# Performance work log

Measured on AMD Instinct MI355X. Metric: run time of the kernel, lower is better.

Reference implementation:

```python
import jax, jax.numpy as jnp
import numpy as np

FILTER_LEN = 32
EXPECTED_SI_POWER_DB = -15
SCALE = float(np.sqrt(10.0 ** (EXPECTED_SI_POWER_DB / 10.0)))  # outputScaleFactor


def _fir(x, k):
    # x: [B,H,W,1], k: [1,FILTER_LEN,1,1]; valid conv along W (matches Conv2D kernel_size=(1,L))
    return jax.lax.conv_general_dilated(
        x, k, window_strides=(1, 1), padding='VALID',
        dimension_numbers=('NHWC', 'HWIO', 'NHWC'))


def setup_inputs() -> dict:
    key = jax.random.key(0)
    ks = jax.random.split(key, 6)
    B, H, W = 16, 64, 16384
    x_real = jax.random.normal(ks[0], (B, H, W, 1), dtype=jnp.float32)
    x_imag = jax.random.normal(ks[1], (B, H, W, 1), dtype=jnp.float32)
    # learned params (Conv2D kernels, HWIO layout, no bias)
    w_nl1 = jax.random.normal(ks[2], (1, 1, 1, 8), dtype=jnp.float32) * 0.5   # layerNL1
    w_nl2 = jax.random.normal(ks[3], (1, 1, 8, 1), dtype=jnp.float32) * 0.5   # layerNL3
    w_lin_real = jax.random.normal(ks[4], (1, FILTER_LEN, 1, 1), dtype=jnp.float32) * 0.1  # layerLIN1
    w_lin_imag = jax.random.normal(ks[5], (1, FILTER_LEN, 1, 1), dtype=jnp.float32) * 0.1  # layerLIN2
    return {'x_real': x_real, 'x_imag': x_imag, 'w_nl1': w_nl1, 'w_nl2': w_nl2,
            'w_lin_real': w_lin_real, 'w_lin_imag': w_lin_imag}


def reference(x_real, x_imag, w_nl1, w_nl2, w_lin_real, w_lin_imag):
    # complex envelope
    x_mag = jnp.sqrt(x_real * x_real + x_imag * x_imag)          # tf.math.abs
    x_phase = jnp.arctan2(x_imag, x_real)                        # tf.math.angle
    # 1x1 conv MLP on magnitude: 1 -> 8 (tanh) -> 1
    h = jnp.tanh(jnp.einsum('bhwc,co->bhwo', x_mag, w_nl1[0, 0]))
    h = jnp.einsum('bhwc,co->bhwo', h, w_nl2[0, 0])
    # re-attach phase
    xr = h * jnp.cos(x_phase)
    xi = h * jnp.sin(x_phase)
    # complex FIR: (lin_real + j*lin_imag) applied to (xr + j*xi)
    yr = _fir(xr, w_lin_real) - _fir(xi, w_lin_imag)
    yi = _fir(xi, w_lin_real) + _fir(xr, w_lin_imag)
    # stack real/imag in last dim (stands in for tf.complex), apply output scale
    return SCALE * jnp.stack([yr, yi], axis=-1)  # [B,H,W-31,1,2]
```

## Files before the change

kernel.cpp:

```cpp
#include <hip/hip_runtime.h>
#include <math.h>

#define W_IN     16384
#define FLT      32
#define W_OUT    (W_IN - FLT + 1)
#define TILE_OUT 2048
#define TILE_IN  (TILE_OUT + FLT)
#define R        8
#define NT       256
#define N_TILES  8
#define LUT_N    2048
#define LUT_MAXM 16.0f
#define LUT_SCL  (LUT_N / LUT_MAXM)
#define OUT_SCALE 0.17782794100389228f

__device__ __forceinline__ int chunk_pf(int c) { return (c + (c >> 3)) << 2; }
#define PAD_CHUNKS (TILE_IN / 4 + TILE_IN / 32 + 1)
#define TILE_FLOATS (PAD_CHUNKS * 4)

__global__ void build_lut_kernel(const float* __restrict__ w1,
                                 const float* __restrict__ w2,
                                 float* __restrict__ lut) {
    const int k = blockIdx.x * blockDim.x + threadIdx.x;
    if (k >= LUT_N) return;
    float c1[8], c2[8];
#pragma unroll
    for (int j = 0; j < 8; ++j) { c1[j] = w1[j]; c2[j] = w2[j]; }
    if (k == 0) {
        float g0 = 0.f;
#pragma unroll
        for (int j = 0; j < 8; ++j) g0 += c2[j] * c1[j];
        lut[0] = g0;
    } else {
        const float m = (float)k * (LUT_MAXM / LUT_N);
        float h = 0.f;
#pragma unroll
        for (int j = 0; j < 8; ++j) h += c2[j] * tanhf(c1[j] * m);
        lut[k] = h / m;
    }
}

__global__ __launch_bounds__(NT, 4)
void fused_env_mlp_fir_kernel(const float* __restrict__ xr,
                              const float* __restrict__ xi,
                              const float* __restrict__ lut_g,
                              const float* __restrict__ wlr,
                              const float* __restrict__ wli,
                              float* __restrict__ out)
{
    __shared__ float slut[LUT_N];
    __shared__ float stile[2 * TILE_FLOATS];
    float* const sxr = stile;
    float* const sxi = stile + TILE_FLOATS;

    const int bid    = blockIdx.x;
    const int row    = bid >> 3;
    const int tile   = bid & 7;
    const int tstart = tile * TILE_OUT;
    const int tid    = threadIdx.x;

#pragma unroll
    for (int i = tid; i < LUT_N / 4; i += NT)
        *(float4*)(slut + i * 4) = *(const float4*)(lut_g + i * 4);
    __syncthreads();

    const float* __restrict__ xr_row = xr + (size_t)row * W_IN;
    const float* __restrict__ xi_row = xi + (size_t)row * W_IN;

    for (int c = tid; c < TILE_IN / 4; c += NT) {
        const int g = tstart + c * 4;
        float4 vr, vi;
        if (g + 3 < W_IN) {
            vr = *(const float4*)(xr_row + g);
            vi = *(const float4*)(xi_row + g);
        } else {
            vr = make_float4(0.f, 0.f, 0.f, 0.f);
            vi = make_float4(0.f, 0.f, 0.f, 0.f);
        }
        float ar[4] = {vr.x, vr.y, vr.z, vr.w};
        float ai[4] = {vi.x, vi.y, vi.z, vi.w};
        float orr[4], oii[4];
#pragma unroll
        for (int e = 0; e < 4; ++e) {
            const float a = ar[e], b = ai[e];
            const float s = fmaxf(fmaf(a, a, b * b), 1e-30f);
            const float rs = rsqrtf(s);
            const float mag  = s * rs;
            const float idxf = mag * LUT_SCL;
            int i = (int)idxf;
            i = min(i, LUT_N - 2);
            const float fr = idxf - (float)i;
            const float g0 = slut[i], g1 = slut[i + 1];
            const float gg = fmaf(fr, g1 - g0, g0);
            orr[e] = a * gg;
            oii[e] = b * gg;
        }
        const int pf = chunk_pf(c);
        *(float4*)(sxr + pf) = make_float4(orr[0], orr[1], orr[2], orr[3]);
        *(float4*)(sxi + pf) = make_float4(oii[0], oii[1], oii[2], oii[3]);
    }
    __syncthreads();

    const int c0 = 2 * tid;
    float4 r0 = *(const float4*)(sxr + chunk_pf(c0 + 0));
    float4 i0 = *(const float4*)(sxi + chunk_pf(c0 + 0));
    float4 r1 = *(const float4*)(sxr + chunk_pf(c0 + 1));
    float4 i1 = *(const float4*)(sxi + chunk_pf(c0 + 1));
    float4 r2 = *(const float4*)(sxr + chunk_pf(c0 + 2));
    float4 i2 = *(const float4*)(sxi + chunk_pf(c0 + 2));

    float accr[R], acci[R];
#pragma unroll
    for (int r = 0; r < R; ++r) { accr[r] = 0.f; acci[r] = 0.f; }

#pragma unroll
    for (int g = 0; g < 8; ++g) {
        const float wa[12] = {r0.x, r0.y, r0.z, r0.w, r1.x, r1.y, r1.z, r1.w,
                              r2.x, r2.y, r2.z, r2.w};
        const float wb[12] = {i0.x, i0.y, i0.z, i0.w, i1.x, i1.y, i1.z, i1.w,
                              i2.x, i2.y, i2.z, i2.w};
#pragma unroll
        for (int kk = 0; kk < 4; ++kk) {
            const int k = 4 * g + kk;
            const float wr = wlr[k];
            const float wi = wli[k];
#pragma unroll
            for (int r = 0; r < R; ++r) {
                const float a = wa[kk + r];
                const float b = wb[kk + r];
                accr[r] = fmaf(a,  wr, accr[r]);
                accr[r] = fmaf(b, -wi, accr[r]);
                acci[r] = fmaf(b,  wr, acci[r]);
                acci[r] = fmaf(a,  wi, acci[r]);
            }
        }
        r0 = r1; r1 = r2; i0 = i1; i1 = i2;
        if (g < 7) {
            r2 = *(const float4*)(sxr + chunk_pf(c0 + g + 3));
            i2 = *(const float4*)(sxi + chunk_pf(c0 + g + 3));
        }
    }

    __syncthreads();
#pragma unroll
    for (int j = 0; j < 4; ++j) {
        float4 v = make_float4(OUT_SCALE * accr[2 * j],
                               OUT_SCALE * acci[2 * j],
                               OUT_SCALE * accr[2 * j + 1],
                               OUT_SCALE * acci[2 * j + 1]);
        *(float4*)(stile + chunk_pf(4 * tid + j)) = v;
    }
    __syncthreads();

    float* __restrict__ out_row = out + (size_t)row * (W_OUT * 2);
    const int remain = W_OUT - tstart;
#pragma unroll
    for (int j = 0; j < 8; ++j) {
        const int u = tid + 256 * j;
        if (u < remain) {
            const float* p = stile + chunk_pf(u >> 1) + 2 * (u & 1);
            *(float2*)(out_row + (size_t)(tstart + u) * 2) =
                make_float2(p[0], p[1]);
        }
    }
}

extern "C" void kernel_launch(void* const* d_in, const int* in_sizes, int n_in,
                              void* d_out, int out_size, void* d_ws, size_t ws_size,
                              hipStream_t stream) {
    const float* xr  = (const float*)d_in[0];
    const float* xi  = (const float*)d_in[1];
    const float* w1  = (const float*)d_in[2];
    const float* w2  = (const float*)d_in[3];
    const float* wlr = (const float*)d_in[4];
    const float* wli = (const float*)d_in[5];
    float* out = (float*)d_out;
    float* lut = (float*)d_ws;

    build_lut_kernel<<<dim3(LUT_N / NT), dim3(NT), 0, stream>>>(w1, w2, lut);

    const int rows = 16 * 64;
    fused_env_mlp_fir_kernel<<<dim3(rows * N_TILES), dim3(NT), 0, stream>>>(
        xr, xi, lut, wlr, wli, out);
}
```

Baseline: 251.1 us.

## Compute complex FIR with bf16x3-split MFMA Toeplitz matmuls instead of scalar FMAs

The 32-tap complex FIR now runs as matrix multiplies on the bf16 MFMA units. The taps are laid out as a Toeplitz matrix, and both the activations and the taps are split into hi/lo bf16 pairs so the result stays close to fp32 accuracy. Shared memory holds swizzled bf16 hi/lo arrays, and the output scale is folded into the taps. Results are written straight from the MFMA accumulators, which removes the staging pass through shared memory and its extra barriers. The cost is more shared-memory traffic for the split planes, extra split arithmetic, and some precision loss from the dropped lo*lo terms.

```diff
diff --git a/kernel.cpp b/kernel.cpp
--- a/kernel.cpp
+++ b/kernel.cpp
@@ -5,8 +5,7 @@
 #define FLT      32
 #define W_OUT    (W_IN - FLT + 1)
 #define TILE_OUT 2048
-#define TILE_IN  (TILE_OUT + FLT)
-#define R        8
+#define TILE_IN  (TILE_OUT + 64)
 #define NT       256
 #define N_TILES  8
 #define LUT_N    2048
@@ -14,9 +13,21 @@
 #define LUT_SCL  (LUT_N / LUT_MAXM)
 #define OUT_SCALE 0.17782794100389228f
 
-__device__ __forceinline__ int chunk_pf(int c) { return (c + (c >> 3)) << 2; }
-#define PAD_CHUNKS (TILE_IN / 4 + TILE_IN / 32 + 1)
-#define TILE_FLOATS (PAD_CHUNKS * 4)
+#define ARR_B (TILE_IN * 2)
+
+typedef short  short8 __attribute__((ext_vector_type(8)));
+typedef float  f32x4  __attribute__((ext_vector_type(4)));
+
+__device__ __forceinline__ int swz16(int b) {
+    return b ^ (((b >> 7) & 7) << 4);
+}
+
+__device__ __forceinline__ void bsplit(float x, unsigned short& h, unsigned short& l) {
+    const unsigned u = __float_as_uint(x);
+    h = (unsigned short)(u >> 16);
+    const float rem = x - __uint_as_float(u & 0xffff0000u);
+    l = (unsigned short)(__float_as_uint(rem) >> 16);
+}
 
 __global__ void build_lut_kernel(const float* __restrict__ w1,
                                  const float* __restrict__ w2,
@@ -39,6 +50,8 @@
         lut[k] = h / m;
     }
 }
+
+#define MFMA(a, b, c) __builtin_amdgcn_mfma_f32_16x16x32_bf16((a), (b), (c), 0, 0, 0)
 
 __global__ __launch_bounds__(NT, 4)
 void fused_env_mlp_fir_kernel(const float* __restrict__ xr,
@@ -48,27 +61,28 @@
                               const float* __restrict__ wli,
                               float* __restrict__ out)
 {
+    __shared__ __align__(16) unsigned short sx[4 * TILE_IN];
     __shared__ float slut[LUT_N];
-    __shared__ float stile[2 * TILE_FLOATS];
-    float* const sxr = stile;
-    float* const sxi = stile + TILE_FLOATS;
+    __shared__ float staps[64];
 
     const int bid    = blockIdx.x;
     const int row    = bid >> 3;
     const int tile   = bid & 7;
     const int tstart = tile * TILE_OUT;
     const int tid    = threadIdx.x;
-
-#pragma unroll
+    const int lane   = tid & 63;
+
     for (int i = tid; i < LUT_N / 4; i += NT)
-        *(float4*)(slut + i * 4) = *(const float4*)(lut_g + i * 4);
+        *(float4*)(slut + 4 * i) = *(const float4*)(lut_g + 4 * i);
+    if (tid < 32)       staps[tid] = wlr[tid] * OUT_SCALE;
+    else if (tid < 64)  staps[tid] = wli[tid - 32] * OUT_SCALE;
     __syncthreads();
 
     const float* __restrict__ xr_row = xr + (size_t)row * W_IN;
     const float* __restrict__ xi_row = xi + (size_t)row * W_IN;
 
     for (int c = tid; c < TILE_IN / 4; c += NT) {
-        const int g = tstart + c * 4;
+        const int g = tstart + 4 * c;
         float4 vr, vi;
         if (g + 3 < W_IN) {
             vr = *(const float4*)(xr_row + g);
@@ -77,9 +91,9 @@
             vr = make_float4(0.f, 0.f, 0.f, 0.f);
             vi = make_float4(0.f, 0.f, 0.f, 0.f);
         }
-        float ar[4] = {vr.x, vr.y, vr.z, vr.w};
-        float ai[4] = {vi.x, vi.y, vi.z, vi.w};
-        float orr[4], oii[4];
+        const float ar[4] = {vr.x, vr.y, vr.z, vr.w};
+        const float ai[4] = {vi.x, vi.y, vi.z, vi.w};
+        unsigned short rha[4], rla[4], iha[4], ila[4];
 #pragma unroll
         for (int e = 0; e < 4; ++e) {
             const float a = ar[e], b = ai[e];
@@ -92,75 +106,93 @@
             const float fr = idxf - (float)i;
             const float g0 = slut[i], g1 = slut[i + 1];
             const float gg = fmaf(fr, g1 - g0, g0);
-            orr[e] = a * gg;
-            oii[e] = b * gg;
-        }
-        const int pf = chunk_pf(c);
-        *(float4*)(sxr + pf) = make_float4(orr[0], orr[1], orr[2], orr[3]);
-        *(float4*)(sxi + pf) = make_float4(oii[0], oii[1], oii[2], oii[3]);
+            bsplit(a * gg, rha[e], rla[e]);
+            bsplit(b * gg, iha[e], ila[e]);
+        }
+        const int pb = swz16(8 * c);
+        char* sb = (char*)sx;
+        *(ushort4*)(sb + 0 * ARR_B + pb) = make_ushort4(rha[0], rha[1], rha[2], rha[3]);
+        *(ushort4*)(sb + 1 * ARR_B + pb) = make_ushort4(rla[0], rla[1], rla[2], rla[3]);
+        *(ushort4*)(sb + 2 * ARR_B + pb) = make_ushort4(iha[0], iha[1], iha[2], iha[3]);
+        *(ushort4*)(sb + 3 * ARR_B + pb) = make_ushort4(ila[0], ila[1], ila[2], ila[3]);
+    }
+
+    short8 frh[2], frl[2], fih[2], fil[2];
+    {
+        const int fm  = lane & 15;
+        const int fk0 = (lane >> 4) << 3;
+#pragma unroll
+        for (int c = 0; c < 2; ++c) {
+#pragma unroll
+            for (int e = 0; e < 8; ++e) {
+                const int t = fk0 + e - fm + 32 * c;
+                const bool v = ((unsigned)t < 32u);
+                const int ti = v ? t : 0;
+                const float fr_ = v ? staps[ti]      : 0.f;
+                const float fi_ = v ? staps[32 + ti] : 0.f;
+                unsigned short h, l;
+                bsplit(fr_, h, l); frh[c][e] = (short)h; frl[c][e] = (short)l;
+                bsplit(fi_, h, l); fih[c][e] = (short)h; fil[c][e] = (short)l;
+            }
+        }
     }
     __syncthreads();
 
-    const int c0 = 2 * tid;
-    float4 r0 = *(const float4*)(sxr + chunk_pf(c0 + 0));
-    float4 i0 = *(const float4*)(sxi + chunk_pf(c0 + 0));
-    float4 r1 = *(const float4*)(sxr + chunk_pf(c0 + 1));
-    float4 i1 = *(const float4*)(sxi + chunk_pf(c0 + 1));
-    float4 r2 = *(const float4*)(sxr + chunk_pf(c0 + 2));
-    float4 i2 = *(const float4*)(sxi + chunk_pf(c0 + 2));
-
-    float accr[R], acci[R];
-#pragma unroll
-    for (int r = 0; r < R; ++r) { accr[r] = 0.f; acci[r] = 0.f; }
-
-#pragma unroll
-    for (int g = 0; g < 8; ++g) {
-        const float wa[12] = {r0.x, r0.y, r0.z, r0.w, r1.x, r1.y, r1.z, r1.w,
-                              r2.x, r2.y, r2.z, r2.w};
-        const float wb[12] = {i0.x, i0.y, i0.z, i0.w, i1.x, i1.y, i1.z, i1.w,
-                              i2.x, i2.y, i2.z, i2.w};
-#pragma unroll
-        for (int kk = 0; kk < 4; ++kk) {
-            const int k = 4 * g + kk;
-            const float wr = wlr[k];
-            const float wi = wli[k];
-#pragma unroll
-            for (int r = 0; r < R; ++r) {
-                const float a = wa[kk + r];
-                const float b = wb[kk + r];
-                accr[r] = fmaf(a,  wr, accr[r]);
-                accr[r] = fmaf(b, -wi, accr[r]);
-                acci[r] = fmaf(b,  wr, acci[r]);
-                acci[r] = fmaf(a,  wi, acci[r]);
-            }
-        }
-        r0 = r1; r1 = r2; i0 = i1; i1 = i2;
-        if (g < 7) {
-            r2 = *(const float4*)(sxr + chunk_pf(c0 + g + 3));
-            i2 = *(const float4*)(sxi + chunk_pf(c0 + g + 3));
-        }
-    }
-
-    __syncthreads();
-#pragma unroll
-    for (int j = 0; j < 4; ++j) {
-        float4 v = make_float4(OUT_SCALE * accr[2 * j],
-                               OUT_SCALE * acci[2 * j],
-                               OUT_SCALE * accr[2 * j + 1],
-                               OUT_SCALE * acci[2 * j + 1]);
-        *(float4*)(stile + chunk_pf(4 * tid + j)) = v;
-    }
-    __syncthreads();
-
+    const int wid = tid >> 6;
+    const int rr  = lane & 15;
+    const int jj  = lane >> 4;
     float* __restrict__ out_row = out + (size_t)row * (W_OUT * 2);
     const int remain = W_OUT - tstart;
-#pragma unroll
-    for (int j = 0; j < 8; ++j) {
-        const int u = tid + 256 * j;
-        if (u < remain) {
-            const float* p = stile + chunk_pf(u >> 1) + 2 * (u & 1);
-            *(float2*)(out_row + (size_t)(tstart + u) * 2) =
-                make_float2(p[0], p[1]);
+    const char* sb = (const char*)sx;
+
+    const short8 sgn = {(short)0x8000, (short)0x8000, (short)0x8000, (short)0x8000,
+                        (short)0x8000, (short)0x8000, (short)0x8000, (short)0x8000};
+
+#pragma unroll
+    for (int gi = 0; gi < 2; ++gi) {
+        const int grp = wid + 4 * gi;
+        const int s   = grp << 8;
+        const int bl = 2 * s + 32 * rr + 16 * jj;
+        const int a0 = swz16(bl);
+        const int a1 = swz16(bl + 64);
+        const short8 xrh0 = *(const short8*)(sb + 0 * ARR_B + a0);
+        const short8 xrh1 = *(const short8*)(sb + 0 * ARR_B + a1);
+        const short8 xrl0 = *(const short8*)(sb + 1 * ARR_B + a0);
+        const short8 xrl1 = *(const short8*)(sb + 1 * ARR_B + a1);
+        const short8 xih0 = *(const short8*)(sb + 2 * ARR_B + a0);
+        const short8 xih1 = *(const short8*)(sb + 2 * ARR_B + a1);
+        const short8 xil0 = *(const short8*)(sb + 3 * ARR_B + a0);
+        const short8 xil1 = *(const short8*)(sb + 3 * ARR_B + a1);
+        const short8 nih0 = xih0 ^ sgn;
+        const short8 nih1 = xih1 ^ sgn;
+        const short8 nil0 = xil0 ^ sgn;
+        const short8 nil1 = xil1 ^ sgn;
+
+        f32x4 accr = {0.f, 0.f, 0.f, 0.f};
+        f32x4 acci = {0.f, 0.f, 0.f, 0.f};
+        accr = MFMA(frh[0], xrh0, accr);  acci = MFMA(frh[0], xih0, acci);
+        accr = MFMA(frh[1], xrh1, accr);  acci = MFMA(frh[1], xih1, acci);
+        accr = MFMA(fih[0], nih0, accr);  acci = MFMA(fih[0], xrh0, acci);
+        accr = MFMA(fih[1], nih1, accr);  acci = MFMA(fih[1], xrh1, acci);
+        accr = MFMA(frh[0], xrl0, accr);  acci = MFMA(frh[0], xil0, acci);
+        accr = MFMA(frh[1], xrl1, accr);  acci = MFMA(frh[1], xil1, acci);
+        accr = MFMA(frl[0], xrh0, accr);  acci = MFMA(frl[0], xih0, acci);
+        accr = MFMA(frl[1], xrh1, accr);  acci = MFMA(frl[1], xih1, acci);
+        accr = MFMA(fih[0], nil0, accr);  acci = MFMA(fih[0], xrl0, acci);
+        accr = MFMA(fih[1], nil1, accr);  acci = MFMA(fih[1], xrl1, acci);
+        accr = MFMA(fil[0], nih0, accr);  acci = MFMA(fil[0], xrh0, acci);
+        accr = MFMA(fil[1], nih1, accr);  acci = MFMA(fil[1], xrh1, acci);
+
+        const int p0 = s + 16 * rr + 4 * jj;
+        float* dst = out_row + (size_t)(tstart + p0) * 2;
+        if (p0 + 3 < remain) {
+            *(float4*)(dst)     = make_float4(accr[0], acci[0], accr[1], acci[1]);
+            *(float4*)(dst + 4) = make_float4(accr[2], acci[2], accr[3], acci[3]);
+        } else {
+#pragma unroll
+            for (int q = 0; q < 4; ++q)
+                if (p0 + q < remain)
+                    *(float2*)(dst + 2 * q) = make_float2(accr[q], acci[q]);
         }
     }
 }
```

Measured after the change: 253.4 us. About the same (+0.9%).
